# Kernel optimization log

Measured on AMD Instinct MI355X. Metric: run time of the kernel, lower is better.

## Reference

```python
import jax, jax.numpy as jnp
import numpy as np

N = 50000
E = 600000
LOOKBACK = 96
HIDDEN = 128
HORIZON = 24
N_LAYERS = 3


def setup_inputs() -> dict:
    key = jax.random.key(0)
    ks = jax.random.split(key, 10)
    x = jax.random.normal(ks[0], (N, LOOKBACK), dtype=jnp.float32)
    y = jax.random.normal(ks[1], (N, HORIZON), dtype=jnp.float32)
    edge_index = jax.random.randint(ks[2], (2, E), 0, N, dtype=jnp.int64)
    s_in = 1.0 / np.sqrt(LOOKBACK)
    W_in = jax.random.uniform(ks[3], (LOOKBACK, HIDDEN), jnp.float32, -s_in, s_in)
    b_in = jax.random.uniform(ks[4], (HIDDEN,), jnp.float32, -s_in, s_in)
    s_h = 1.0 / np.sqrt(HIDDEN)
    Ws = jax.random.uniform(ks[5], (N_LAYERS, HIDDEN, HIDDEN), jnp.float32, -s_h, s_h)
    bs = jnp.zeros((N_LAYERS, HIDDEN), dtype=jnp.float32)
    W_out = jax.random.uniform(ks[6], (HIDDEN, HORIZON), jnp.float32, -s_h, s_h)
    b_out = jax.random.uniform(ks[7], (HORIZON,), jnp.float32, -s_h, s_h)
    return {"x": x, "y": y, "edge_index": edge_index, "W_in": W_in,
            "b_in": b_in, "Ws": Ws, "bs": bs, "W_out": W_out, "b_out": b_out}


def _gcn_conv(h, W, b, src, dst, norm):
    # h: [N, D]; PyG GCNConv: out = D^{-1/2}(A+I)D^{-1/2} (h W) + b
    hw = h @ W                                    # [N, D]
    msg = hw[src] * norm[:, None]                 # [E+N, D] gather + scale
    out = jnp.zeros_like(hw).at[dst].add(msg)     # scatter-add aggregation
    return out + b


def reference(x, y, edge_index, W_in, b_in, Ws, bs, W_out, b_out):
    n = x.shape[0]
    # add self loops (PyG GCNConv default)
    loop = jnp.arange(n, dtype=edge_index.dtype)
    src = jnp.concatenate([edge_index[0], loop])
    dst = jnp.concatenate([edge_index[1], loop])
    # symmetric normalization: deg over destination, norm = d^-1/2[src]*d^-1/2[dst]
    deg = jnp.zeros((n,), dtype=x.dtype).at[dst].add(1.0)
    dinv = jnp.where(deg > 0, jax.lax.rsqrt(deg), 0.0)
    norm = dinv[src] * dinv[dst]                  # [E+N]

    h = x @ W_in + b_in                           # input projection
    for l in range(Ws.shape[0]):
        h = _gcn_conv(h, Ws[l], bs[l], src, dst, norm)
        h = jax.nn.relu(h)
    out = h @ W_out + b_out                       # [N, horizon]
    return (out, y)
```

## Files before the change

kernel.cpp:

```cpp
#include <hip/hip_runtime.h>
#include <hip/hip_bf16.h>
#include <hip/hip_fp8.h>

#define LOOKBACK 96
#define HID 128
#define HORIZON 24
#define NLAYERS 3
#define CHUNK 2048

typedef __attribute__((ext_vector_type(8))) short short8v;
typedef __attribute__((ext_vector_type(4))) float f32x4;

__device__ __forceinline__ ushort f2bf(float f) {
    __hip_bfloat16 h = __float2bfloat16(f);
    return *(ushort*)&h;
}

__device__ __forceinline__ void f8acc(uint w, float* a) {
    __hip_fp8_e4m3 h0, h1, h2, h3;
    h0.__x = (unsigned char)(w & 0xff);
    h1.__x = (unsigned char)((w >> 8) & 0xff);
    h2.__x = (unsigned char)((w >> 16) & 0xff);
    h3.__x = (unsigned char)(w >> 24);
    a[0] += (float)h0; a[1] += (float)h1; a[2] += (float)h2; a[3] += (float)h3;
}
__device__ __forceinline__ uint f8enc4(float a, float b, float c, float d) {
    __hip_fp8_e4m3 ha(a), hb(b), hc(c), hd(d);
    return (uint)ha.__x | ((uint)hb.__x << 8) | ((uint)hc.__x << 16) | ((uint)hd.__x << 24);
}

__global__ void wprep_k(const float* __restrict__ W_in, const float* __restrict__ Ws,
                        const float* __restrict__ W_out,
                        ushort* __restrict__ WinT, ushort* __restrict__ WsT,
                        ushort* __restrict__ WoutT) {
    int idx = blockIdx.x * 256 + threadIdx.x;
    if (idx < 12288) {
        int k = idx / 128, c = idx % 128;
        WinT[c * 96 + k] = f2bf(W_in[idx]);
    } else if (idx < 61440) {
        int r = idx - 12288;
        int l = r / 16384, q = r % 16384;
        int k = q / 128, c = q % 128;
        WsT[l * 16384 + c * 128 + k] = f2bf(Ws[r]);
    } else if (idx < 64512) {
        int r = idx - 61440;
        int k = r / 24, c = r % 24;
        WoutT[c * 128 + k] = f2bf(W_out[r]);
    } else {
        WoutT[3072 + (idx - 64512)] = 0;
    }
}

__global__ __launch_bounds__(256) void rhist_k(
    const int* __restrict__ dst, int* __restrict__ bh,
    uchar* __restrict__ z8row, int E, int NB)
{
    __shared__ int hist[256];
    int t = threadIdx.x, b = blockIdx.x;
    int gid = b * 256 + t;
    if (gid < 32) ((uint*)z8row)[gid] = 0;
    hist[t] = 0;
    __syncthreads();
    int base = b * CHUNK;
    #pragma unroll
    for (int i = 0; i < CHUNK / 256; ++i) {
        int e = base + i * 256 + t;
        if (e < E) atomicAdd(&hist[(dst[e] >> 8) & 255], 1);
    }
    __syncthreads();
    bh[t * NB + b] = hist[t];
}

__global__ __launch_bounds__(1024) void rscan2_k(const int* __restrict__ bh,
                                                 int* __restrict__ bh2, int M) {
    __shared__ int s[1024];
    __shared__ int base_s;
    int t = threadIdx.x, b = blockIdx.x;
    int acc = 0;
    for (int i = t; i < b * 1024; i += 1024) acc += bh[i];
    s[t] = acc;
    __syncthreads();
    for (int off = 512; off > 0; off >>= 1) {
        if (t < off) s[t] += s[t + off];
        __syncthreads();
    }
    if (t == 0) base_s = s[0];
    __syncthreads();
    int i = b * 1024 + t;
    int v = (i < M) ? bh[i] : 0;
    s[t] = v;
    __syncthreads();
    for (int off = 1; off < 1024; off <<= 1) {
        int xx = s[t];
        int yy = (t >= off) ? s[t - off] : 0;
        __syncthreads();
        s[t] = xx + yy;
        __syncthreads();
    }
    if (i < M) bh2[i] = base_s + s[t] - v;
}

__global__ __launch_bounds__(256) void rscatter_k(
    const int* __restrict__ src, const int* __restrict__ dst,
    const int* __restrict__ bh2, uint* __restrict__ recs, int E, int NB)
{
    __shared__ int basearr[256];
    __shared__ int cnt[256];
    int t = threadIdx.x, b = blockIdx.x;
    basearr[t] = bh2[t * NB + b];
    cnt[t] = 0;
    __syncthreads();
    int base = b * CHUNK;
    #pragma unroll
    for (int i = 0; i < CHUNK / 256; ++i) {
        int e = base + i * 256 + t;
        if (e < E) {
            int d = dst[e];
            int dg = (d >> 8) & 255;
            int r = atomicAdd(&cnt[dg], 1);
            recs[basearr[dg] + r] = ((uint)d << 16) | (uint)src[e];
        }
    }
}

__global__ __launch_bounds__(1024) void rbucket_k(
    const uint* __restrict__ recs, const int* __restrict__ bh2,
    int* __restrict__ srcs, int* __restrict__ offsets, float* __restrict__ dinv,
    int n, int E, int NB, int NBK)
{
    __shared__ uint lrec[4096];
    __shared__ int hist[256], loff[256], cnt[256], tmp[256];
    int t = threadIdx.x, b = blockIdx.x;
    int start = bh2[b * NB];
    int end = (b + 1 < NBK) ? bh2[(b + 1) * NB] : E;
    int L = end - start;
    if (L > 4096) L = 4096;
    if (t < 256) { hist[t] = 0; cnt[t] = 0; }
    __syncthreads();
    #pragma unroll
    for (int i = 0; i < 4; ++i) {
        int j = i * 1024 + t;
        if (j < L) {
            uint r = recs[start + j];
            lrec[j] = r;
            atomicAdd(&hist[(r >> 16) & 255], 1);
        }
    }
    __syncthreads();
    if (t < 256) tmp[t] = hist[t];
    __syncthreads();
    for (int off = 1; off < 256; off <<= 1) {
        int v = 0;
        if (t < 256) { v = tmp[t]; if (t >= off) v += tmp[t - off]; }
        __syncthreads();
        if (t < 256) tmp[t] = v;
        __syncthreads();
    }
    if (t < 256) loff[t] = tmp[t] - hist[t];
    __syncthreads();
    #pragma unroll
    for (int i = 0; i < 4; ++i) {
        int j = i * 1024 + t;
        if (j < L) {
            uint r = lrec[j];
            int lo = (r >> 16) & 255;
            int pos = start + loff[lo] + atomicAdd(&cnt[lo], 1);
            srcs[pos] = (int)(r & 0xffffu);
        }
    }
    if (t < 256) {
        int d = b * 256 + t;
        if (d <= n) {
            int o = start + loff[t];
            if (d < n) {
                offsets[d] = o;
                dinv[d] = rsqrtf((float)hist[t] + 1.0f);
            } else {
                offsets[n] = o;
            }
        }
    }
}

__global__ __launch_bounds__(256) void agg_k(
    const uchar* __restrict__ zh8, ushort* __restrict__ out,
    const float* __restrict__ dinv,
    const int* __restrict__ offsets, const int* __restrict__ srcs,
    const float* __restrict__ bias, int n)
{
    int node = (blockIdx.x * 256 + threadIdx.x) >> 6;
    if (node >= n) return;
    node = __builtin_amdgcn_readfirstlane(node);
    const int lane = threadIdx.x & 63;
    const int g = lane >> 3;
    const int f = lane & 7;

    const int off = offsets[node];
    const int cnt = offsets[node + 1] - off;
    const int* ep = srcs + off;
    const float di = dinv[node];

    float acc[16];
    #pragma unroll
    for (int j = 0; j < 16; ++j) acc[j] = 0.0f;
    {
        int s = (g == 0) ? node : n;
        uint4 u = *(const uint4*)&zh8[(size_t)s * HID + f * 16];
        f8acc(u.x, acc + 0); f8acc(u.y, acc + 4);
        f8acc(u.z, acc + 8); f8acc(u.w, acc + 12);
    }

    #pragma unroll 2
    for (int i = 0; i < cnt; i += 8) {
        int idx = ep[i + g];
        int s = (i + g < cnt) ? idx : n;
        uint4 u = *(const uint4*)&zh8[(size_t)s * HID + f * 16];
        f8acc(u.x, acc + 0); f8acc(u.y, acc + 4);
        f8acc(u.z, acc + 8); f8acc(u.w, acc + 12);
    }

    #pragma unroll
    for (int j = 0; j < 16; ++j) {
        acc[j] += __shfl_xor(acc[j], 8);
        acc[j] += __shfl_xor(acc[j], 16);
        acc[j] += __shfl_xor(acc[j], 32);
    }

    if (g == 0) {
        const int c0 = f * 16;
        float r[16];
        #pragma unroll
        for (int j = 0; j < 16; j += 4) {
            float4 bv = *(const float4*)&bias[c0 + j];
            r[j + 0] = fmaxf(fmaf(di, acc[j + 0], bv.x), 0.0f);
            r[j + 1] = fmaxf(fmaf(di, acc[j + 1], bv.y), 0.0f);
            r[j + 2] = fmaxf(fmaf(di, acc[j + 2], bv.z), 0.0f);
            r[j + 3] = fmaxf(fmaf(di, acc[j + 3], bv.w), 0.0f);
        }
        uint pw[8];
        #pragma unroll
        for (int j = 0; j < 8; ++j)
            pw[j] = (uint)f2bf(r[2 * j]) | ((uint)f2bf(r[2 * j + 1]) << 16);
        *(uint4*)&out[(size_t)node * HID + c0] = make_uint4(pw[0], pw[1], pw[2], pw[3]);
        *(uint4*)&out[(size_t)node * HID + c0 + 8] = make_uint4(pw[4], pw[5], pw[6], pw[7]);
    }
}

template <int K, bool AF32, bool BIAS, bool SCALE, bool F8>
__global__ __launch_bounds__(256) void mfma_gemm_k(
    const void* __restrict__ Araw, const ushort* __restrict__ BT,
    const float* __restrict__ bias, const float* __restrict__ dinv,
    ushort* __restrict__ C, uchar* __restrict__ C8, int n)
{
    constexpr int KSTEPS = K / 32;
    constexpr int PAD = K + 8;
    __shared__ ushort Bt[128][PAD];

    const int tid = threadIdx.x;
    const int wid = tid >> 6;
    const int lane = tid & 63;
    const int brow = blockIdx.x * 64;

    constexpr int NV = K * 16;
    #pragma unroll
    for (int i = tid; i < NV; i += 256) {
        int col = (i * 8) / K;
        int k0 = (i * 8) % K;
        *(short8v*)&Bt[col][k0] = *(const short8v*)&BT[(size_t)i * 8];
    }
    __syncthreads();

    const int arow = brow + wid * 16 + (lane & 15);
    const int rowc = (arow < n) ? arow : (n - 1);
    const int kb = (lane >> 4) * 8;

    f32x4 acc[8];
    #pragma unroll
    for (int j = 0; j < 8; ++j) acc[j] = (f32x4){0.f, 0.f, 0.f, 0.f};

    #pragma unroll
    for (int kt = 0; kt < KSTEPS; ++kt) {
        short8v a;
        if (AF32) {
            const float* ap = (const float*)Araw + (size_t)rowc * K + kt * 32 + kb;
            float4 f0 = *(const float4*)ap;
            float4 f1 = *(const float4*)(ap + 4);
            a[0] = (short)f2bf(f0.x); a[1] = (short)f2bf(f0.y);
            a[2] = (short)f2bf(f0.z); a[3] = (short)f2bf(f0.w);
            a[4] = (short)f2bf(f1.x); a[5] = (short)f2bf(f1.y);
            a[6] = (short)f2bf(f1.z); a[7] = (short)f2bf(f1.w);
        } else {
            a = *(const short8v*)((const ushort*)Araw + (size_t)rowc * K + kt * 32 + kb);
        }
        #pragma unroll
        for (int j = 0; j < 8; ++j) {
            short8v b = *(const short8v*)&Bt[j * 16 + (lane & 15)][kt * 32 + kb];
            acc[j] = __builtin_amdgcn_mfma_f32_16x16x32_bf16(a, b, acc[j], 0, 0, 0);
        }
    }

    const int r0l = wid * 16 + (lane >> 4) * 4;
    float dsc[4];
    if (SCALE) {
        #pragma unroll
        for (int r = 0; r < 4; ++r)
            dsc[r] = (brow + r0l + r < n) ? dinv[brow + r0l + r] : 0.0f;
    }
    __syncthreads();
    ushort* Cs = &Bt[0][0];
    const int cl = lane & 15;
    #pragma unroll
    for (int j = 0; j < 8; ++j) {
        int col = j * 16 + cl;
        float bv = BIAS ? bias[col] : 0.0f;
        #pragma unroll
        for (int r = 0; r < 4; ++r) {
            float v = acc[j][r];
            if (SCALE) v *= dsc[r];
            if (BIAS) v += bv;
            Cs[(r0l + r) * 136 + col] = f2bf(v);
        }
    }
    __syncthreads();
    int lrow = tid >> 2;
    int seg = (tid & 3) * 32;
    int grow = brow + lrow;
    if (grow < n) {
        uint pw[8];
        #pragma unroll
        for (int q = 0; q < 4; ++q) {
            short8v v = *(const short8v*)&Cs[lrow * 136 + seg + q * 8];
            if (!F8) {
                *(short8v*)&C[(size_t)grow * HID + seg + q * 8] = v;
            } else {
                float fv[8];
                #pragma unroll
                for (int j = 0; j < 8; ++j)
                    fv[j] = __uint_as_float(((uint)(ushort)v[j]) << 16);
                pw[2 * q]     = f8enc4(fv[0], fv[1], fv[2], fv[3]);
                pw[2 * q + 1] = f8enc4(fv[4], fv[5], fv[6], fv[7]);
            }
        }
        if (F8) {
            *(uint4*)&C8[(size_t)grow * HID + seg]      = make_uint4(pw[0], pw[1], pw[2], pw[3]);
            *(uint4*)&C8[(size_t)grow * HID + seg + 16] = make_uint4(pw[4], pw[5], pw[6], pw[7]);
        }
    }
}

__global__ __launch_bounds__(256) void gemm_out_k(
    const ushort* __restrict__ A, const ushort* __restrict__ BT,
    const float* __restrict__ bias, const float* __restrict__ y,
    float* __restrict__ out, float* __restrict__ ycopy, int n)
{
    const int tid = threadIdx.x;
    const int wid = tid >> 6;
    const int lane = tid & 63;
    const int brow = blockIdx.x * 64;
    const int arow = brow + wid * 16 + (lane & 15);
    const int rowc = (arow < n) ? arow : (n - 1);
    const int kb = (lane >> 4) * 8;

    f32x4 acc[2];
    acc[0] = (f32x4){0.f, 0.f, 0.f, 0.f};
    acc[1] = (f32x4){0.f, 0.f, 0.f, 0.f};

    #pragma unroll
    for (int kt = 0; kt < 4; ++kt) {
        short8v a = *(const short8v*)(A + (size_t)rowc * HID + kt * 32 + kb);
        #pragma unroll
        for (int j = 0; j < 2; ++j) {
            short8v b = *(const short8v*)&BT[(size_t)(j * 16 + (lane & 15)) * HID + kt * 32 + kb];
            acc[j] = __builtin_amdgcn_mfma_f32_16x16x32_bf16(a, b, acc[j], 0, 0, 0);
        }
    }

    const int r0 = brow + wid * 16 + (lane >> 4) * 4;
    const int cl = lane & 15;
    #pragma unroll
    for (int j = 0; j < 2; ++j) {
        int col = j * 16 + cl;
        if (col < HORIZON) {
            float bv = bias[col];
            #pragma unroll
            for (int r = 0; r < 4; ++r) {
                int row = r0 + r;
                if (row < n) out[(size_t)row * HORIZON + col] = acc[j][r] + bv;
            }
        }
    }

    const float4* y4 = (const float4*)y;
    float4* o4 = (float4*)ycopy;
    const int lim = n * 6;
    int base = blockIdx.x * 384;
    for (int t = tid; t < 384; t += 256) {
        int i = base + t;
        if (i < lim) o4[i] = y4[i];
    }
}

extern "C" void kernel_launch(void* const* d_in, const int* in_sizes, int n_in,
                              void* d_out, int out_size, void* d_ws, size_t ws_size,
                              hipStream_t stream) {
    const float* x     = (const float*)d_in[0];
    const float* y     = (const float*)d_in[1];
    const int*   ei    = (const int*)d_in[2];
    const float* W_in  = (const float*)d_in[3];
    const float* b_in  = (const float*)d_in[4];
    const float* Ws    = (const float*)d_in[5];
    const float* bs    = (const float*)d_in[6];
    const float* W_out = (const float*)d_in[7];
    const float* b_out = (const float*)d_in[8];
    float* out = (float*)d_out;

    const int n = in_sizes[0] / LOOKBACK;
    const int E = in_sizes[2] / 2;
    const int* src = ei;
    const int* dst = ei + E;

    const int NB  = (E + CHUNK - 1) / CHUNK;
    const int M   = 256 * NB;
    const int nsb = (M + 1023) / 1024;
    const int NBK = (n >> 8) + 1;

    char* p = (char*)d_ws;
    auto alloc = [&](size_t bytes) { char* q = p; p += (bytes + 15) & ~(size_t)15; return q; };
    float*  dinv    = (float*)alloc((size_t)n * 4);
    int*    offsets = (int*)alloc((size_t)(n + 4) * 4);
    int*    bh      = (int*)alloc((size_t)M * 4);
    int*    bh2     = (int*)alloc((size_t)M * 4);
    uint*   recs    = (uint*)alloc((size_t)E * 4);
    int*    srcs    = (int*)alloc((size_t)(E + 16) * 4);
    ushort* WinT    = (ushort*)alloc((size_t)128 * 96 * 2);
    ushort* WsT     = (ushort*)alloc((size_t)NLAYERS * 128 * 128 * 2);
    ushort* WoutT   = (ushort*)alloc((size_t)32 * 128 * 2);
    ushort* bufA    = (ushort*)alloc((size_t)(n + 1) * HID * 2);
    uchar*  bufB8   = (uchar*)alloc((size_t)(n + 1) * HID);

    wprep_k<<<256, 256, 0, stream>>>(W_in, Ws, W_out, WinT, WsT, WoutT);
    rhist_k<<<NB, 256, 0, stream>>>(dst, bh, bufB8 + (size_t)n * HID, E, NB);
    rscan2_k<<<nsb, 1024, 0, stream>>>(bh, bh2, M);
    rscatter_k<<<NB, 256, 0, stream>>>(src, dst, bh2, recs, E, NB);
    rbucket_k<<<NBK, 1024, 0, stream>>>(recs, bh2, srcs, offsets, dinv, n, E, NB, NBK);

    const int gemm_grid = (n + 63) / 64;
    mfma_gemm_k<LOOKBACK, true, true, false, false><<<gemm_grid, 256, 0, stream>>>(
        x, WinT, b_in, nullptr, bufA, nullptr, n);

    const int agg_grid = (n * 64 + 255) / 256;
    for (int l = 0; l < NLAYERS; ++l) {
        mfma_gemm_k<HID, false, false, true, true><<<gemm_grid, 256, 0, stream>>>(
            bufA, WsT + (size_t)l * HID * HID, nullptr, dinv, nullptr, bufB8, n);
        agg_k<<<agg_grid, 256, 0, stream>>>(bufB8, bufA, dinv, offsets,
                                            srcs, bs + (size_t)l * HID, n);
    }

    gemm_out_k<<<gemm_grid, 256, 0, stream>>>(bufA, WoutT, b_out, y,
                                              out, out + (size_t)n * HORIZON, n);
}
```

Baseline: 188.3 us.

## Split aggregation into two feature-half passes with two nodes per wavefront

```diff
diff --git a/kernel.cpp b/kernel.cpp
--- a/kernel.cpp
+++ b/kernel.cpp
@@ -182,52 +182,56 @@
     }
 }
 
-__global__ __launch_bounds__(256) void agg_k(
+__global__ __launch_bounds__(256) void agg_half_k(
     const uchar* __restrict__ zh8, ushort* __restrict__ out,
     const float* __restrict__ dinv,
     const int* __restrict__ offsets, const int* __restrict__ srcs,
-    const float* __restrict__ bias, int n)
-{
-    int node = (blockIdx.x * 256 + threadIdx.x) >> 6;
-    if (node >= n) return;
-    node = __builtin_amdgcn_readfirstlane(node);
+    const float* __restrict__ bias, int n, int h)
+{
+    const int wv = (blockIdx.x * 256 + threadIdx.x) >> 6;
     const int lane = threadIdx.x & 63;
-    const int g = lane >> 3;
-    const int f = lane & 7;
-
-    const int off = offsets[node];
-    const int cnt = offsets[node + 1] - off;
+    const int half = lane >> 5;
+    const int l5 = lane & 31;
+    const int g = l5 >> 2;
+    const int f = l5 & 3;
+    const int node = wv * 2 + half;
+    const bool valid = node < n;
+    const int nodec = valid ? node : (n - 1);
+
+    const int off = offsets[nodec];
+    const int cnt = valid ? (offsets[nodec + 1] - off) : 0;
     const int* ep = srcs + off;
-    const float di = dinv[node];
+    const float di = dinv[nodec];
+    const int c0 = h * 64 + f * 16;
 
     float acc[16];
     #pragma unroll
     for (int j = 0; j < 16; ++j) acc[j] = 0.0f;
     {
-        int s = (g == 0) ? node : n;
-        uint4 u = *(const uint4*)&zh8[(size_t)s * HID + f * 16];
+        int s = (g == 0 && valid) ? nodec : n;
+        uint4 u = *(const uint4*)&zh8[(size_t)s * HID + c0];
         f8acc(u.x, acc + 0); f8acc(u.y, acc + 4);
         f8acc(u.z, acc + 8); f8acc(u.w, acc + 12);
     }
 
-    #pragma unroll 2
-    for (int i = 0; i < cnt; i += 8) {
+    int cm = cnt;
+    cm = max(cm, __shfl_xor(cm, 32));
+    for (int i = 0; i < cm; i += 8) {
         int idx = ep[i + g];
         int s = (i + g < cnt) ? idx : n;
-        uint4 u = *(const uint4*)&zh8[(size_t)s * HID + f * 16];
+        uint4 u = *(const uint4*)&zh8[(size_t)s * HID + c0];
         f8acc(u.x, acc + 0); f8acc(u.y, acc + 4);
         f8acc(u.z, acc + 8); f8acc(u.w, acc + 12);
     }
 
     #pragma unroll
     for (int j = 0; j < 16; ++j) {
+        acc[j] += __shfl_xor(acc[j], 4);
         acc[j] += __shfl_xor(acc[j], 8);
         acc[j] += __shfl_xor(acc[j], 16);
-        acc[j] += __shfl_xor(acc[j], 32);
-    }
-
-    if (g == 0) {
-        const int c0 = f * 16;
+    }
+
+    if (g == 0 && valid) {
         float r[16];
         #pragma unroll
         for (int j = 0; j < 16; j += 4) {
@@ -448,12 +452,15 @@
     mfma_gemm_k<LOOKBACK, true, true, false, false><<<gemm_grid, 256, 0, stream>>>(
         x, WinT, b_in, nullptr, bufA, nullptr, n);
 
-    const int agg_grid = (n * 64 + 255) / 256;
+    const int nwaves = (n + 1) / 2;
+    const int aggh_grid = (nwaves + 3) / 4;
     for (int l = 0; l < NLAYERS; ++l) {
         mfma_gemm_k<HID, false, false, true, true><<<gemm_grid, 256, 0, stream>>>(
             bufA, WsT + (size_t)l * HID * HID, nullptr, dinv, nullptr, bufB8, n);
-        agg_k<<<agg_grid, 256, 0, stream>>>(bufB8, bufA, dinv, offsets,
-                                            srcs, bs + (size_t)l * HID, n);
+        agg_half_k<<<aggh_grid, 256, 0, stream>>>(bufB8, bufA, dinv, offsets,
+                                                  srcs, bs + (size_t)l * HID, n, 0);
+        agg_half_k<<<aggh_grid, 256, 0, stream>>>(bufB8, bufA, dinv, offsets,
+                                                  srcs, bs + (size_t)l * HID, n, 1);
     }
 
     gemm_out_k<<<gemm_grid, 256, 0, stream>>>(bufA, WoutT, b_out, y,
```

After: 225.6 us. +19.8%, slower.
